# Kernel tuning notes

Hardware: AMD Instinct MI355X
Metric: run time of the kernel (lower is better)

Reference implementation:

```python
import jax, jax.numpy as jnp
import numpy as np

D_MODEL = 1024
D_STATE = 64
D_CONV = 4
EXPAND = 2
HEADDIM = 64  # Hydra default (config.headdim is not forwarded by the block)
D_INNER = EXPAND * D_MODEL            # 2048
NHEADS = D_INNER // HEADDIM           # 32
D_IN_PROJ = 2 * D_INNER + 2 * D_STATE + 2 * NHEADS  # 4288
CONV_DIM = D_INNER + 2 * D_STATE      # 2176
CHUNK = 64
EPS = 1e-5
BATCH, SEQLEN = 4, 2048


def setup_inputs() -> dict:
    key = jax.random.key(0)
    ks = jax.random.split(key, 8)
    w = lambda k, shape, s=0.02: (jax.random.normal(k, shape, jnp.float32) * s)
    dt = jnp.linspace(1e-3, 1e-1, NHEADS, dtype=jnp.float32)
    return {
        "hidden_states": jax.random.normal(ks[0], (BATCH, SEQLEN, D_MODEL), jnp.float32),
        "residual": jax.random.normal(ks[1], (BATCH, SEQLEN, D_MODEL), jnp.float32),
        "norm_weight": jnp.ones((D_MODEL,), jnp.float32),
        "in_proj_w": w(ks[2], (D_IN_PROJ, D_MODEL)),
        "conv_w": w(ks[3], (CONV_DIM, 1, D_CONV), 0.2),
        "conv_b": jnp.zeros((CONV_DIM,), jnp.float32),
        "dt_bias": jnp.log(jnp.expm1(dt)),  # inverse-softplus init, as in Mamba2/Hydra
        "A_log": jnp.log(jnp.linspace(1.0, 16.0, NHEADS, dtype=jnp.float32)),
        "D": jnp.ones((NHEADS,), jnp.float32),
        "fc_D_w": w(ks[4], (NHEADS, D_INNER)),
        "gn_weight": jnp.ones((D_INNER,), jnp.float32),
        "out_proj_w": w(ks[5], (D_MODEL, D_INNER)),
    }


def _rmsnorm(x, weight):
    x = x.astype(jnp.float32)
    return x * jax.lax.rsqrt(jnp.mean(x * x, axis=-1, keepdims=True) + EPS) * weight


def _segsum(x):
    # x: (..., T) -> lower-triangular cumulative segment sums, -inf above diag
    T = x.shape[-1]
    cs = jnp.cumsum(x, axis=-1)
    ss = cs[..., :, None] - cs[..., None, :]
    mask = jnp.tril(jnp.ones((T, T), bool))
    return jnp.where(mask, ss, -jnp.inf)


def _ssd(X, A, Bm, Cm, block):
    # Chunked SSD (mamba_chunk_scan_combined math, D=None, z=None, ngroups=1)
    # X: (b,l,h,p) = dt*x ; A: (b,l,h) = dt*A ; Bm, Cm: (b,l,n)
    b, l, h, p = X.shape
    c = l // block
    X = X.reshape(b, c, block, h, p)
    A = A.reshape(b, c, block, h).transpose(0, 3, 1, 2)          # (b,h,c,l)
    Bm = Bm.reshape(b, c, block, -1)
    Cm = Cm.reshape(b, c, block, -1)
    A_cum = jnp.cumsum(A, axis=-1)
    Lmat = jnp.exp(_segsum(A))                                   # (b,h,c,l,s)
    Y_diag = jnp.einsum("bcln,bcsn,bhcls,bcshp->bclhp", Cm, Bm, Lmat, X)
    decay = jnp.exp(A_cum[..., -1:] - A_cum)                     # (b,h,c,l)
    states = jnp.einsum("bcln,bhcl,bclhp->bchpn", Bm, decay, X)
    states = jnp.concatenate([jnp.zeros_like(states[:, :1]), states], axis=1)
    dchunk = jnp.exp(_segsum(jnp.pad(A_cum[..., -1], ((0, 0), (0, 0), (1, 0)))))
    states = jnp.einsum("bhzc,bchpn->bzhpn", dchunk, states)[:, :-1]
    Y_off = jnp.einsum("bcln,bchpn,bhcl->bclhp", Cm, states, jnp.exp(A_cum))
    return (Y_diag + Y_off).reshape(b, l, h, p)


def _hydra(h, in_proj_w, conv_w, conv_b, dt_bias, A_log, D, fc_D_w, gn_weight, out_proj_w):
    b, l, _ = h.shape
    zxbcdt = h @ in_proj_w.T                                     # (b,l,4288)
    z = zxbcdt[..., :D_INNER]
    xBC = zxbcdt[..., D_INNER:D_INNER + CONV_DIM]
    dt = zxbcdt[..., D_INNER + CONV_DIM:]                        # (b,l,2H)
    # fwd heads + time-flipped bwd heads, stacked on batch -> (2b,l,H)
    dt = jnp.concatenate([dt[..., :NHEADS], jnp.flip(dt[..., NHEADS:], axis=1)], axis=0)
    dt = jax.nn.softplus(dt + dt_bias)
    A = -jnp.exp(A_log)                                          # (H,)
    # causal depthwise conv, kernel D_CONV
    pad = jnp.pad(xBC, ((0, 0), (D_CONV - 1, 0), (0, 0)))
    conv = conv_b + sum(pad[:, k:k + l, :] * conv_w[:, 0, k] for k in range(D_CONV))
    xBC = jax.nn.silu(conv)
    x = xBC[..., :D_INNER]
    Bm = xBC[..., D_INNER:D_INNER + D_STATE]
    Cm = xBC[..., D_INNER + D_STATE:]
    x2 = jnp.concatenate([x, jnp.flip(x, axis=1)], axis=0)       # (2b,l,d_inner)
    B2 = jnp.concatenate([Bm, jnp.flip(Bm, axis=1)], axis=0)
    C2 = jnp.concatenate([Cm, jnp.flip(Cm, axis=1)], axis=0)
    X = x2.reshape(2 * b, l, NHEADS, HEADDIM) * dt[..., None]    # dt-discretized input
    y = _ssd(X, dt * A, B2, C2, CHUNK).reshape(2 * b, l, D_INNER)
    # quasiseparable combine: strict lower (shift fwd by +1) + strict upper + data-dep diag
    y = jnp.roll(y, 1, axis=1).at[:, 0, :].set(0.0)
    y = y[:b] + jnp.flip(y[b:], axis=1)
    Deff = x @ fc_D_w.T + D                                      # (b,l,H)
    y = y + x * jnp.repeat(Deff, HEADDIM, axis=-1)
    y = _rmsnorm(y * jax.nn.silu(z), gn_weight)                  # gated RMSNorm
    return y @ out_proj_w.T


def reference(hidden_states, residual, norm_weight, in_proj_w, conv_w, conv_b,
              dt_bias, A_log, D, fc_D_w, gn_weight, out_proj_w):
    res = (hidden_states + residual).astype(jnp.float32)         # residual_in_fp32
    h = _rmsnorm(res, norm_weight)                               # fused add+RMSNorm (prenorm)
    out = _hydra(h, in_proj_w, conv_w, conv_b, dt_bias, A_log, D, fc_D_w, gn_weight, out_proj_w)
    return out, res
```

## Files before the change

kernel.cpp:

```cpp
#include <hip/hip_runtime.h>

typedef __attribute__((ext_vector_type(4))) float f32x4;
typedef __attribute__((ext_vector_type(8))) short short8;
typedef __attribute__((ext_vector_type(8))) unsigned short ushort8;
typedef unsigned short u16;
typedef unsigned int u32;

#define DMODEL 1024
#define DINNER 2048
#define NH     32
#define DIP    4288
#define DIP_PAD 4352
#define CONVD  2176
#define LSEQ   2048
#define ROWS   8192
#define NCHUNK 32

static __device__ __forceinline__ float bf2f(u16 u) {
  u32 x = ((u32)u) << 16;
  return __builtin_bit_cast(float, x);
}
static __device__ __forceinline__ u16 f2bf(float f) {
  u32 x = __builtin_bit_cast(u32, f);
  x += 0x7fffu + ((x >> 16) & 1u);
  return (u16)(x >> 16);
}
static __device__ __forceinline__ f32x4 mfma16(short8 a, short8 b, f32x4 c) {
  return __builtin_amdgcn_mfma_f32_16x16x32_bf16(a, b, c, 0, 0, 0);
}

#define GLDS(gp, lp)                                                     \
  __builtin_amdgcn_global_load_lds(                                     \
      (const __attribute__((address_space(1))) void*)(gp),              \
      (__attribute__((address_space(3))) void*)(lp), 16, 0, 0)

__global__ __launch_bounds__(256) void k_cast(const float* __restrict__ s, u16* __restrict__ d) {
  size_t i = ((size_t)blockIdx.x * 256 + threadIdx.x) * 4;
  float4 v = *(const float4*)(s + i);
  u32 lo = (u32)f2bf(v.x) | ((u32)f2bf(v.y) << 16);
  u32 hi = (u32)f2bf(v.z) | ((u32)f2bf(v.w) << 16);
  *(uint2*)(d + i) = make_uint2(lo, hi);
}

__global__ __launch_bounds__(256) void k_addnorm(const float* __restrict__ h,
                                                 const float* __restrict__ r,
                                                 const float* __restrict__ nw,
                                                 float* __restrict__ res,
                                                 u16* __restrict__ hn) {
  int row = blockIdx.x, t = threadIdx.x;
  const float4* hp = (const float4*)(h + (size_t)row * DMODEL);
  const float4* rp = (const float4*)(r + (size_t)row * DMODEL);
  float4 a = hp[t], b = rp[t];
  float4 s;
  s.x = a.x + b.x; s.y = a.y + b.y; s.z = a.z + b.z; s.w = a.w + b.w;
  ((float4*)(res + (size_t)row * DMODEL))[t] = s;
  float ss = s.x * s.x + s.y * s.y + s.z * s.z + s.w * s.w;
  for (int m = 32; m; m >>= 1) ss += __shfl_xor(ss, m);
  __shared__ float wsum[4];
  if ((t & 63) == 0) wsum[t >> 6] = ss;
  __syncthreads();
  float tot = wsum[0] + wsum[1] + wsum[2] + wsum[3];
  float rinv = rsqrtf(tot * (1.0f / DMODEL) + 1e-5f);
  float4 w4 = ((const float4*)nw)[t];
  u32 lo = (u32)f2bf(s.x * rinv * w4.x) | ((u32)f2bf(s.y * rinv * w4.y) << 16);
  u32 hi = (u32)f2bf(s.z * rinv * w4.z) | ((u32)f2bf(s.w * rinv * w4.w) << 16);
  *(uint2*)(hn + (size_t)row * DMODEL + t * 4) = make_uint2(lo, hi);
}

template <int MODE>
__global__ __launch_bounds__(256) void k_gemm(const u16* __restrict__ A,
                                              const u16* __restrict__ Bw, int K, int nN,
                                              float* __restrict__ outf,
                                              u16* __restrict__ zb, u16* __restrict__ xb,
                                              float* __restrict__ dtp,
                                              const float* __restrict__ dt_bias) {
  constexpr int ABY = 128 * 64 * 2;
  constexpr int TB = 2 * ABY;
  __shared__ char lds[2 * TB];

  const int tid = threadIdx.x, wave = tid >> 6, lane = tid & 63;
  const int wm = wave >> 1, wn = wave & 1;
  const int lr = lane & 15, lg = lane >> 4;

  const int cpx = gridDim.x >> 3;
  const int orig = blockIdx.x;
  const int wg = (orig & 7) * cpx + (orig >> 3);
  const int brow = (wg / nN) * 128;
  const int bcol = (wg % nN) * 128;
  const int NK = K >> 6;

  size_t srcA[4], srcB[4];
#pragma unroll
  for (int g = 0; g < 4; ++g) {
    int d = g * 4096 + tid * 16;
    int s = d ^ (((d >> 7) & 7) << 4);
    srcA[g] = (size_t)(brow + (s >> 7)) * K + ((s & 127) >> 1);
    srcB[g] = (size_t)(bcol + (s >> 7)) * K + ((s & 127) >> 1);
  }

  auto STAGE = [&](int buf, int kt) {
    char* base = lds + buf * TB;
    size_t koff = (size_t)kt * 64;
#pragma unroll
    for (int g = 0; g < 4; ++g)
      GLDS(A + srcA[g] + koff, base + g * 4096 + wave * 1024);
#pragma unroll
    for (int g = 0; g < 4; ++g)
      GLDS(Bw + srcB[g] + koff, base + ABY + g * 4096 + wave * 1024);
  };

  int offA[4][2], offB[4][2];
#pragma unroll
  for (int i = 0; i < 4; ++i)
#pragma unroll
    for (int ks = 0; ks < 2; ++ks) {
      int rA = wm * 64 + i * 16 + lr;
      offA[i][ks] = (rA * 128 + ks * 64 + lg * 16) ^ ((lr & 7) << 4);
      int rB = wn * 64 + i * 16 + lr;
      offB[i][ks] = ABY + ((rB * 128 + ks * 64 + lg * 16) ^ ((lr & 7) << 4));
    }

  f32x4 acc[4][4] = {};
  STAGE(0, 0);
  asm volatile("s_waitcnt vmcnt(0)" ::: "memory");
  __builtin_amdgcn_s_barrier();
  for (int t = 0; t < NK; ++t) {
    const int cur = t & 1;
    if (t + 1 < NK) STAGE(cur ^ 1, t + 1);
    const char* bb = lds + cur * TB;
    short8 af[4], bfr[4];
#pragma unroll
    for (int i = 0; i < 4; ++i) af[i] = *(const short8*)(bb + offA[i][0]);
#pragma unroll
    for (int j = 0; j < 4; ++j) bfr[j] = *(const short8*)(bb + offB[j][0]);
    __builtin_amdgcn_s_setprio(1);
#pragma unroll
    for (int i = 0; i < 4; ++i)
#pragma unroll
      for (int j = 0; j < 4; ++j) acc[i][j] = mfma16(af[i], bfr[j], acc[i][j]);
    __builtin_amdgcn_s_setprio(0);
#pragma unroll
    for (int i = 0; i < 4; ++i) af[i] = *(const short8*)(bb + offA[i][1]);
#pragma unroll
    for (int j = 0; j < 4; ++j) bfr[j] = *(const short8*)(bb + offB[j][1]);
    __builtin_amdgcn_s_setprio(1);
#pragma unroll
    for (int i = 0; i < 4; ++i)
#pragma unroll
      for (int j = 0; j < 4; ++j) acc[i][j] = mfma16(af[i], bfr[j], acc[i][j]);
    __builtin_amdgcn_s_setprio(0);
    if (t + 1 < NK) {
      asm volatile("s_waitcnt vmcnt(0)" ::: "memory");
      __builtin_amdgcn_s_barrier();
    }
  }

  const int mb = brow + wm * 64 + lg * 4;
  const int nb = bcol + wn * 64 + lr;
#pragma unroll
  for (int i = 0; i < 4; ++i)
#pragma unroll
    for (int j = 0; j < 4; ++j)
#pragma unroll
      for (int rr = 0; rr < 4; ++rr) {
        int m = mb + i * 16 + rr;
        int n = nb + j * 16;
        float v = acc[i][j][rr];
        if constexpr (MODE == 1) {
          outf[(size_t)m * 1024 + n] = v;
        } else {
          if (n < DINNER) {
            zb[(size_t)m * DINNER + n] = f2bf(v);
          } else if (n < DINNER + CONVD) {
            xb[(size_t)m * CONVD + (n - DINNER)] = f2bf(v);
          } else if (n < DIP) {
            int h2 = n - (DINNER + CONVD);
            float uu = v + dt_bias[h2 & 31];
            float sp = (uu > 20.f) ? uu : log1pf(expf(uu));
            int bb2 = m >> 11, tt = m & 2047;
            int obb = bb2, ot = tt;
            if (h2 >= 32) { obb = bb2 + 4; ot = 2047 - tt; }
            dtp[((size_t)(obb << 11) + ot) * NH + (h2 & 31)] = sp;
          }
        }
      }
}

__global__ __launch_bounds__(256) void k_conv(const u16* __restrict__ xbc,
                                              const float* __restrict__ cw,
                                              const float* __restrict__ cb,
                                              u16* __restrict__ xc, u16* __restrict__ bm,
                                              u16* __restrict__ cm) {
  int e = blockIdx.x * 256 + threadIdx.x;
  int c8 = e % 272;
  int rq = e / 272;
  int b = rq >> 9;
  int t0 = (rq & 511) * 4;
  int c = c8 * 8;

  float4 w[8];
  float a[4][8];
#pragma unroll
  for (int j = 0; j < 8; ++j) {
    w[j] = *(const float4*)&cw[(c + j) * 4];
    float bias = cb[c + j];
#pragma unroll
    for (int i = 0; i < 4; ++i) a[i][j] = bias;
  }
  const u16* base = xbc + (size_t)(b << 11) * CONVD + c;
#pragma unroll
  for (int k = 0; k < 7; ++k) {
    int tt = t0 - 3 + k;
    if (tt >= 0) {
      ushort8 v = *(const ushort8*)(base + (size_t)tt * CONVD);
#pragma unroll
      for (int i = 0; i < 4; ++i) {
        int kk = k - i;
        if (kk >= 0 && kk < 4) {
#pragma unroll
          for (int j = 0; j < 8; ++j) a[i][j] += bf2f(v[j]) * ((const float*)&w[j])[kk];
        }
      }
    }
  }
#pragma unroll
  for (int i = 0; i < 4; ++i) {
    ushort8 o;
#pragma unroll
    for (int j = 0; j < 8; ++j) {
      float s = a[i][j] * (1.f / (1.f + expf(-a[i][j])));
      o[j] = f2bf(s);
    }
    size_t r = (size_t)(b << 11) + t0 + i;
    if (c8 < 256) *(ushort8*)(xc + r * DINNER + c) = o;
    else if (c8 < 264) *(ushort8*)(bm + r * 64 + (c - DINNER)) = o;
    else *(ushort8*)(cm + r * 64 + (c - DINNER - 64)) = o;
  }
}

__global__ __launch_bounds__(512) void k_ssd(const u16* __restrict__ xc,
                                             const u16* __restrict__ bmat,
                                             const u16* __restrict__ cmat,
                                             const float* __restrict__ dtp,
                                             const float* __restrict__ alog,
                                             u16* __restrict__ y0, u16* __restrict__ y1) {
  const int h = blockIdx.x & 31;
  const int grp = blockIdx.x >> 5;
  const int dir = grp >> 2;
  const int bt = grp & 3;
  const int tid = threadIdx.x, wave = tid >> 6, lane = tid & 63;
  const int lq = wave >> 1, wh = wave & 1;
  const int lr = lane & 15, lg = lane >> 4;
  const float Ah = -expf(alog[h]);

  __shared__ u16 sB[64][72];
  __shared__ u16 sC[64][72];
  __shared__ u16 sXM[64][72];
  __shared__ u16 sXT[64][72];
  __shared__ u16 sBT[64][72];
  __shared__ u16 sSb[64][72];
  __shared__ float sS[64][68];
  __shared__ float sAc[64], sEA[64], sSc[64], sDt[64];

  for (int i = tid; i < 64 * 64; i += 512) {
    sS[i >> 6][i & 63] = 0.f;
    sSb[i >> 6][i & 63] = 0;
  }

  const int srow = tid >> 3, q8 = (tid & 7) * 8;

  auto rowOf = [&](int c) {
    int tdir = c * 64 + srow;
    return bt * LSEQ + (dir ? (LSEQ - 1 - tdir) : tdir);
  };

  int rg = rowOf(0);
  ushort8 rB = *(const ushort8*)(bmat + (size_t)rg * 64 + q8);
  ushort8 rC = *(const ushort8*)(cmat + (size_t)rg * 64 + q8);
  ushort8 rX = *(const ushort8*)(xc + (size_t)rg * DINNER + h * 64 + q8);

  for (int c = 0; c < NCHUNK; ++c) {
    *(ushort8*)&sB[srow][q8] = rB;
    *(ushort8*)&sC[srow][q8] = rC;
    *(ushort8*)&sXM[srow][q8] = rX;
    __syncthreads();

    {
      ushort8 vx, vb;
#pragma unroll
      for (int i = 0; i < 8; ++i) {
        vx[i] = sXM[wave * 8 + i][lane];
        vb[i] = sB[wave * 8 + i][lane];
      }
      *(ushort8*)&sXT[lane][wave * 8] = vx;
      *(ushort8*)&sBT[lane][wave * 8] = vb;
    }
    if (wave == 0) {
      int s = lane;
      float dv = dtp[((size_t)grp * LSEQ + c * 64 + s) * NH + h];
      float a = dv * Ah;
      float x = a;
#pragma unroll
      for (int d = 1; d < 64; d <<= 1) {
        float y = __shfl_up(x, d);
        if (s >= d) x += y;
      }
      float tot = __shfl(x, 63);
      sAc[s] = x;
      sEA[s] = expf(x);
      sSc[s] = expf(tot - x) * dv;
      sDt[s] = dv;
    }
    __syncthreads();

    if (c + 1 < NCHUNK) {
      int rg2 = rowOf(c + 1);
      rB = *(const ushort8*)(bmat + (size_t)rg2 * 64 + q8);
      rC = *(const ushort8*)(cmat + (size_t)rg2 * 64 + q8);
      rX = *(const ushort8*)(xc + (size_t)rg2 * DINNER + h * 64 + q8);
    }

    f32x4 acc_y[2] = {};
    {
      f32x4 acc_g[2] = {};
#pragma unroll
      for (int ks = 0; ks < 2; ++ks) {
        int kof = ks * 32 + lg * 8;
        short8 af = *(const short8*)&sC[lq * 16 + lr][kof];
#pragma unroll
        for (int nt = 0; nt < 2; ++nt) {
          short8 bf = *(const short8*)&sB[wh * 32 + nt * 16 + lr][kof];
          acc_g[nt] = mfma16(af, bf, acc_g[nt]);
        }
      }
#pragma unroll
      for (int ks = 0; ks < 2; ++ks) {
        int kof = ks * 32 + lg * 8;
        short8 af = *(const short8*)&sC[lq * 16 + lr][kof];
#pragma unroll
        for (int nt = 0; nt < 2; ++nt) {
          short8 bf = *(const short8*)&sSb[wh * 32 + nt * 16 + lr][kof];
          acc_y[nt] = mfma16(af, bf, acc_y[nt]);
        }
      }
#pragma unroll
      for (int nt = 0; nt < 2; ++nt)
#pragma unroll
        for (int rr = 0; rr < 4; ++rr) {
          int l = lq * 16 + lg * 4 + rr;
          int s = wh * 32 + nt * 16 + lr;
          float g = acc_g[nt][rr];
          float m = (l >= s) ? g * sDt[s] * expf(sAc[l] - sAc[s]) : 0.f;
          sXM[l][s] = f2bf(m);
        }
    }
    __syncthreads();

#pragma unroll
    for (int nt = 0; nt < 2; ++nt)
#pragma unroll
      for (int rr = 0; rr < 4; ++rr) acc_y[nt][rr] *= sEA[lq * 16 + lg * 4 + rr];
#pragma unroll
    for (int ks = 0; ks < 2; ++ks) {
      int kof = ks * 32 + lg * 8;
      short8 af = *(const short8*)&sXM[lq * 16 + lr][kof];
#pragma unroll
      for (int nt = 0; nt < 2; ++nt) {
        short8 bf = *(const short8*)&sXT[wh * 32 + nt * 16 + lr][kof];
        acc_y[nt] = mfma16(af, bf, acc_y[nt]);
      }
    }
#pragma unroll
    for (int nt = 0; nt < 2; ++nt)
#pragma unroll
      for (int rr = 0; rr < 4; ++rr) {
        int l = lq * 16 + lg * 4 + rr;
        int p = wh * 32 + nt * 16 + lr;
        int tg = c * 64 + l;
        if (tg <= LSEQ - 2) {
          float v = acc_y[nt][rr];
          if (dir == 0)
            y0[((size_t)bt * LSEQ + tg + 1) * DINNER + h * 64 + p] = f2bf(v);
          else
            y1[((size_t)bt * LSEQ + (LSEQ - 2 - tg)) * DINNER + h * 64 + p] = f2bf(v);
        }
      }
    if (c == 0 && tid < 64) {
      if (dir == 0)
        y0[((size_t)bt * LSEQ) * DINNER + h * 64 + tid] = 0;
      else
        y1[((size_t)bt * LSEQ + (LSEQ - 1)) * DINNER + h * 64 + tid] = 0;
    }
    {
      f32x4 acc_s[2] = {};
#pragma unroll
      for (int ks = 0; ks < 2; ++ks) {
        int kof = ks * 32 + lg * 8;
        ushort8 xr = *(const ushort8*)&sXT[lq * 16 + lr][kof];
        short8 af;
#pragma unroll
        for (int e = 0; e < 8; ++e) af[e] = (short)f2bf(bf2f(xr[e]) * sSc[kof + e]);
#pragma unroll
        for (int nt = 0; nt < 2; ++nt) {
          short8 bf = *(const short8*)&sBT[wh * 32 + nt * 16 + lr][kof];
          acc_s[nt] = mfma16(af, bf, acc_s[nt]);
        }
      }
      float lam = sEA[63];
#pragma unroll
      for (int nt = 0; nt < 2; ++nt)
#pragma unroll
        for (int rr = 0; rr < 4; ++rr) {
          int p = lq * 16 + lg * 4 + rr;
          int n = wh * 32 + nt * 16 + lr;
          float ns = lam * sS[p][n] + acc_s[nt][rr];
          sS[p][n] = ns;
          sSb[p][n] = f2bf(ns);
        }
    }
    __syncthreads();
  }
}

__global__ __launch_bounds__(256) void k_deff(const u16* __restrict__ xcv,
                                              const u16* __restrict__ fwb,
                                              const float* __restrict__ Dv,
                                              float* __restrict__ deff) {
  __shared__ float red[2][64][8];
  const int tid = threadIdx.x, wave = tid >> 6, lane = tid & 63;
  const int lr = lane & 15, lg = lane >> 4;
  const int rowg = wave & 1;
  const int kg = wave >> 1;
  const int rb = blockIdx.x * 32 + rowg * 16;
  const u16* xrow = xcv + (size_t)(rb + lr) * DINNER + kg * 1024 + lg * 8;
  const u16* f0 = fwb + (size_t)lr * DINNER + kg * 1024 + lg * 8;
  const u16* f1 = fwb + (size_t)(16 + lr) * DINNER + kg * 1024 + lg * 8;
  f32x4 a0 = {}, a1 = {};
  for (int k = 0; k < 1024; k += 32) {
    short8 bf = *(const short8*)(xrow + k);
    short8 af0 = *(const short8*)(f0 + k);
    short8 af1 = *(const short8*)(f1 + k);
    a0 = mfma16(af0, bf, a0);
    a1 = mfma16(af1, bf, a1);
  }
  if (kg == 1) {
#pragma unroll
    for (int rr = 0; rr < 4; ++rr) {
      red[rowg][lane][rr] = a0[rr];
      red[rowg][lane][4 + rr] = a1[rr];
    }
  }
  __syncthreads();
  if (kg == 0) {
    float4 o0, o1;
#pragma unroll
    for (int rr = 0; rr < 4; ++rr) {
      ((float*)&o0)[rr] = a0[rr] + red[rowg][lane][rr] + Dv[lg * 4 + rr];
      ((float*)&o1)[rr] = a1[rr] + red[rowg][lane][4 + rr] + Dv[16 + lg * 4 + rr];
    }
    *(float4*)&deff[(size_t)(rb + lr) * NH + lg * 4] = o0;
    *(float4*)&deff[(size_t)(rb + lr) * NH + 16 + lg * 4] = o1;
  }
}

__global__ __launch_bounds__(256) void k_gate(const u16* __restrict__ yb0,
                                              const u16* __restrict__ yb1,
                                              const u16* __restrict__ xcv,
                                              const float* __restrict__ deff,
                                              const u16* __restrict__ zb,
                                              const float* __restrict__ gnw,
                                              u16* __restrict__ yn) {
  int row = blockIdx.x, t = threadIdx.x;
  size_t base = (size_t)row * DINNER + t * 8;
  ushort8 y0v = *(const ushort8*)(yb0 + base);
  ushort8 y1v = *(const ushort8*)(yb1 + base);
  ushort8 xv = *(const ushort8*)(xcv + base);
  ushort8 zv = *(const ushort8*)(zb + base);
  float de = deff[row * NH + (t >> 3)];
  float g[8];
  float ss = 0.f;
#pragma unroll
  for (int j = 0; j < 8; ++j) {
    float y = bf2f(y0v[j]) + bf2f(y1v[j]) + bf2f(xv[j]) * de;
    float z = bf2f(zv[j]);
    float gg = y * (z / (1.f + expf(-z)));
    g[j] = gg;
    ss += gg * gg;
  }
  for (int m = 32; m; m >>= 1) ss += __shfl_xor(ss, m);
  __shared__ float wsum[4];
  if ((t & 63) == 0) wsum[t >> 6] = ss;
  __syncthreads();
  float tot = wsum[0] + wsum[1] + wsum[2] + wsum[3];
  float rinv = rsqrtf(tot * (1.0f / DINNER) + 1e-5f);
  u32 w0 = (u32)f2bf(g[0] * rinv * gnw[t * 8 + 0]) | ((u32)f2bf(g[1] * rinv * gnw[t * 8 + 1]) << 16);
  u32 w1 = (u32)f2bf(g[2] * rinv * gnw[t * 8 + 2]) | ((u32)f2bf(g[3] * rinv * gnw[t * 8 + 3]) << 16);
  u32 w2 = (u32)f2bf(g[4] * rinv * gnw[t * 8 + 4]) | ((u32)f2bf(g[5] * rinv * gnw[t * 8 + 5]) << 16);
  u32 w3 = (u32)f2bf(g[6] * rinv * gnw[t * 8 + 6]) | ((u32)f2bf(g[7] * rinv * gnw[t * 8 + 7]) << 16);
  *(uint4*)(yn + base) = make_uint4(w0, w1, w2, w3);
}

extern "C" void kernel_launch(void* const* d_in, const int* in_sizes, int n_in,
                              void* d_out, int out_size, void* d_ws, size_t ws_size,
                              hipStream_t stream) {
  (void)in_sizes; (void)n_in; (void)out_size; (void)ws_size;
  const float* hid = (const float*)d_in[0];
  const float* resin = (const float*)d_in[1];
  const float* nw = (const float*)d_in[2];
  const float* w1 = (const float*)d_in[3];
  const float* cw = (const float*)d_in[4];
  const float* cb = (const float*)d_in[5];
  const float* dtb = (const float*)d_in[6];
  const float* alog = (const float*)d_in[7];
  const float* Dv = (const float*)d_in[8];
  const float* fcw = (const float*)d_in[9];
  const float* gnw = (const float*)d_in[10];
  const float* w2 = (const float*)d_in[11];
  float* out = (float*)d_out;
  float* resout = out + (size_t)ROWS * DMODEL;

  char* ws = (char*)d_ws;
  size_t o = 0;
  auto alloc = [&](size_t bytes) {
    char* p = ws + o;
    o += (bytes + 255) & ~(size_t)255;
    return p;
  };
  u16* W1b = (u16*)alloc((size_t)DIP_PAD * DMODEL * 2);
  u16* HN = (u16*)alloc((size_t)ROWS * DMODEL * 2);
  u16* XBC = (u16*)alloc((size_t)ROWS * CONVD * 2);
  u16* ZB = (u16*)alloc((size_t)ROWS * DINNER * 2);
  u16* XC = (u16*)alloc((size_t)ROWS * DINNER * 2);
  u16* BM = (u16*)alloc((size_t)ROWS * 64 * 2);
  u16* CM = (u16*)alloc((size_t)ROWS * 64 * 2);
  float* DT = (float*)alloc((size_t)8 * LSEQ * NH * 4);
  float* DE = (float*)alloc((size_t)ROWS * NH * 4);
  u16* FWB = (u16*)alloc((size_t)NH * DINNER * 2);
  u16* YB0 = XBC;
  u16* YB1 = (u16*)out;
  u16* W2b = W1b;
  u16* YN = HN;

  k_cast<<<(DIP * DMODEL) / 1024, 256, 0, stream>>>(w1, W1b);
  k_addnorm<<<ROWS, 256, 0, stream>>>(hid, resin, nw, resout, HN);
  k_gemm<0><<<64 * 34, 256, 0, stream>>>(HN, W1b, DMODEL, 34, nullptr, ZB, XBC, DT, dtb);
  k_conv<<<(ROWS / 4) * 272 / 256, 256, 0, stream>>>(XBC, cw, cb, XC, BM, CM);
  k_ssd<<<256, 512, 0, stream>>>(XC, BM, CM, DT, alog, YB0, YB1);
  k_cast<<<(DMODEL * DINNER) / 1024, 256, 0, stream>>>(w2, W2b);
  k_cast<<<(NH * DINNER) / 1024, 256, 0, stream>>>(fcw, FWB);
  k_deff<<<ROWS / 32, 256, 0, stream>>>(XC, FWB, Dv, DE);
  k_gate<<<ROWS, 256, 0, stream>>>(YB0, YB1, XC, DE, ZB, gnw, YN);
  k_gemm<1><<<64 * 8, 256, 0, stream>>>(YN, W2b, DINNER, 8, out, nullptr, nullptr, nullptr,
                                        nullptr);
}
```

Measured before the change: 412.9 us.

## Use 256x256-tile, 8-wave GEMM for the input projection

Adds a dedicated in_proj GEMM kernel with 256x256 output tiles, 512 threads and 128KB LDS double buffering. The K-tile is split into two halves, and loads for the next tile are interleaved with MFMA phases. The larger tile raises arithmetic intensity and cuts global/LDS traffic per FLOP. The cost is a single block per CU and fewer blocks overall (544), which can hurt tail balance and latency hiding. The out_proj GEMM keeps the old 128x128 kernel, now specialized to the fp32 output path.

```diff
diff --git a/kernel.cpp b/kernel.cpp
--- a/kernel.cpp
+++ b/kernel.cpp
@@ -67,13 +67,157 @@
   *(uint2*)(hn + (size_t)row * DMODEL + t * 4) = make_uint2(lo, hi);
 }
 
-template <int MODE>
+__global__ __launch_bounds__(512) void k_gemm256(const u16* __restrict__ A,
+                                                 const u16* __restrict__ Bw, int K, int nN,
+                                                 u16* __restrict__ zb, u16* __restrict__ xb,
+                                                 float* __restrict__ dtp,
+                                                 const float* __restrict__ dt_bias) {
+  __shared__ char lds[131072];
+  const int tid = threadIdx.x, wave = tid >> 6, lane = tid & 63;
+  const int wm = wave >> 2, wn = wave & 3;
+  const int lr = lane & 15, lg = lane >> 4;
+
+  const int cpx = gridDim.x >> 3;
+  const int orig = blockIdx.x;
+  const int wg = (orig & 7) * cpx + (orig >> 3);
+  const int brow = (wg / nN) * 256;
+  const int bcol = (wg % nN) * 256;
+  const int NT = K >> 6;
+
+  size_t srcA[2], srcB[2];
+#pragma unroll
+  for (int g = 0; g < 2; ++g) {
+    int d = g * 8192 + tid * 16;
+    int r = d >> 6;
+    int q = ((d >> 4) & 3) ^ (r & 3);
+    srcA[g] = (size_t)(brow + r) * K + q * 8;
+    srcB[g] = (size_t)(bcol + r) * K + q * 8;
+  }
+
+  auto STAGE_A = [&](int buf, int kh, int kt) {
+    char* dst = lds + buf * 65536 + kh * 16384 + wave * 1024;
+    size_t koff = (size_t)kt * 64 + kh * 32;
+    GLDS(A + srcA[0] + koff, dst);
+    GLDS(A + srcA[1] + koff, dst + 8192);
+  };
+  auto STAGE_B = [&](int buf, int kh, int kt) {
+    char* dst = lds + buf * 65536 + 32768 + kh * 16384 + wave * 1024;
+    size_t koff = (size_t)kt * 64 + kh * 32;
+    GLDS(Bw + srcB[0] + koff, dst);
+    GLDS(Bw + srcB[1] + koff, dst + 8192);
+  };
+
+  int offA[8], offB[4];
+#pragma unroll
+  for (int i = 0; i < 8; ++i) {
+    int row = wm * 128 + i * 16 + lr;
+    offA[i] = row * 64 + ((lg * 16) ^ ((row & 3) << 4));
+  }
+#pragma unroll
+  for (int j = 0; j < 4; ++j) {
+    int row = wn * 64 + j * 16 + lr;
+    offB[j] = 32768 + row * 64 + ((lg * 16) ^ ((row & 3) << 4));
+  }
+
+  f32x4 acc[8][4] = {};
+  STAGE_A(0, 0, 0);
+  STAGE_B(0, 0, 0);
+  STAGE_A(0, 1, 0);
+  STAGE_B(0, 1, 0);
+
+  for (int t = 0; t < NT; ++t) {
+    const int cb = t & 1, nb = cb ^ 1;
+    const char* rb = lds + cb * 65536;
+    short8 af[8], b0, b1;
+    asm volatile("s_waitcnt vmcnt(4)" ::: "memory");
+    __builtin_amdgcn_s_barrier();
+    __builtin_amdgcn_sched_barrier(0);
+#pragma unroll
+    for (int i = 0; i < 8; ++i) af[i] = *(const short8*)(rb + offA[i]);
+    b0 = *(const short8*)(rb + offB[0]);
+    b1 = *(const short8*)(rb + offB[1]);
+    if (t + 1 < NT) STAGE_A(nb, 0, t + 1);
+    __builtin_amdgcn_s_setprio(1);
+#pragma unroll
+    for (int i = 0; i < 8; ++i) {
+      acc[i][0] = mfma16(af[i], b0, acc[i][0]);
+      acc[i][1] = mfma16(af[i], b1, acc[i][1]);
+    }
+    __builtin_amdgcn_s_setprio(0);
+    __builtin_amdgcn_sched_barrier(0);
+    b0 = *(const short8*)(rb + offB[2]);
+    b1 = *(const short8*)(rb + offB[3]);
+    if (t + 1 < NT) STAGE_B(nb, 0, t + 1);
+    __builtin_amdgcn_s_setprio(1);
+#pragma unroll
+    for (int i = 0; i < 8; ++i) {
+      acc[i][2] = mfma16(af[i], b0, acc[i][2]);
+      acc[i][3] = mfma16(af[i], b1, acc[i][3]);
+    }
+    __builtin_amdgcn_s_setprio(0);
+    __builtin_amdgcn_sched_barrier(0);
+    if (t + 1 < NT)
+      asm volatile("s_waitcnt vmcnt(4)" ::: "memory");
+    else
+      asm volatile("s_waitcnt vmcnt(0)" ::: "memory");
+    __builtin_amdgcn_s_barrier();
+    __builtin_amdgcn_sched_barrier(0);
+#pragma unroll
+    for (int i = 0; i < 8; ++i) af[i] = *(const short8*)(rb + 16384 + offA[i]);
+    b0 = *(const short8*)(rb + 16384 + offB[0]);
+    b1 = *(const short8*)(rb + 16384 + offB[1]);
+    if (t + 1 < NT) STAGE_A(nb, 1, t + 1);
+    __builtin_amdgcn_s_setprio(1);
+#pragma unroll
+    for (int i = 0; i < 8; ++i) {
+      acc[i][0] = mfma16(af[i], b0, acc[i][0]);
+      acc[i][1] = mfma16(af[i], b1, acc[i][1]);
+    }
+    __builtin_amdgcn_s_setprio(0);
+    __builtin_amdgcn_sched_barrier(0);
+    b0 = *(const short8*)(rb + 16384 + offB[2]);
+    b1 = *(const short8*)(rb + 16384 + offB[3]);
+    if (t + 1 < NT) STAGE_B(nb, 1, t + 1);
+    __builtin_amdgcn_s_setprio(1);
+#pragma unroll
+    for (int i = 0; i < 8; ++i) {
+      acc[i][2] = mfma16(af[i], b0, acc[i][2]);
+      acc[i][3] = mfma16(af[i], b1, acc[i][3]);
+    }
+    __builtin_amdgcn_s_setprio(0);
+    __builtin_amdgcn_sched_barrier(0);
+  }
+
+  const int mb = brow + wm * 128 + lg * 4;
+  const int nb2 = bcol + wn * 64 + lr;
+#pragma unroll
+  for (int i = 0; i < 8; ++i)
+#pragma unroll
+    for (int j = 0; j < 4; ++j)
+#pragma unroll
+      for (int rr = 0; rr < 4; ++rr) {
+        int m = mb + i * 16 + rr;
+        int n = nb2 + j * 16;
+        float v = acc[i][j][rr];
+        if (n < DINNER) {
+          zb[(size_t)m * DINNER + n] = f2bf(v);
+        } else if (n < DINNER + CONVD) {
+          xb[(size_t)m * CONVD + (n - DINNER)] = f2bf(v);
+        } else if (n < DIP) {
+          int h2 = n - (DINNER + CONVD);
+          float uu = v + dt_bias[h2 & 31];
+          float sp = (uu > 20.f) ? uu : log1pf(expf(uu));
+          int bb2 = m >> 11, tt = m & 2047;
+          int obb = bb2, ot = tt;
+          if (h2 >= 32) { obb = bb2 + 4; ot = 2047 - tt; }
+          dtp[((size_t)(obb << 11) + ot) * NH + (h2 & 31)] = sp;
+        }
+      }
+}
+
 __global__ __launch_bounds__(256) void k_gemm(const u16* __restrict__ A,
                                               const u16* __restrict__ Bw, int K, int nN,
-                                              float* __restrict__ outf,
-                                              u16* __restrict__ zb, u16* __restrict__ xb,
-                                              float* __restrict__ dtp,
-                                              const float* __restrict__ dt_bias) {
+                                              float* __restrict__ outf) {
   constexpr int ABY = 128 * 64 * 2;
   constexpr int TB = 2 * ABY;
   __shared__ char lds[2 * TB];
@@ -165,24 +309,7 @@
       for (int rr = 0; rr < 4; ++rr) {
         int m = mb + i * 16 + rr;
         int n = nb + j * 16;
-        float v = acc[i][j][rr];
-        if constexpr (MODE == 1) {
-          outf[(size_t)m * 1024 + n] = v;
-        } else {
-          if (n < DINNER) {
-            zb[(size_t)m * DINNER + n] = f2bf(v);
-          } else if (n < DINNER + CONVD) {
-            xb[(size_t)m * CONVD + (n - DINNER)] = f2bf(v);
-          } else if (n < DIP) {
-            int h2 = n - (DINNER + CONVD);
-            float uu = v + dt_bias[h2 & 31];
-            float sp = (uu > 20.f) ? uu : log1pf(expf(uu));
-            int bb2 = m >> 11, tt = m & 2047;
-            int obb = bb2, ot = tt;
-            if (h2 >= 32) { obb = bb2 + 4; ot = 2047 - tt; }
-            dtp[((size_t)(obb << 11) + ot) * NH + (h2 & 31)] = sp;
-          }
-        }
+        outf[(size_t)m * 1024 + n] = acc[i][j][rr];
       }
 }
 
@@ -543,13 +670,12 @@
 
   k_cast<<<(DIP * DMODEL) / 1024, 256, 0, stream>>>(w1, W1b);
   k_addnorm<<<ROWS, 256, 0, stream>>>(hid, resin, nw, resout, HN);
-  k_gemm<0><<<64 * 34, 256, 0, stream>>>(HN, W1b, DMODEL, 34, nullptr, ZB, XBC, DT, dtb);
+  k_gemm256<<<32 * 17, 512, 0, stream>>>(HN, W1b, DMODEL, 17, ZB, XBC, DT, dtb);
   k_conv<<<(ROWS / 4) * 272 / 256, 256, 0, stream>>>(XBC, cw, cb, XC, BM, CM);
   k_ssd<<<256, 512, 0, stream>>>(XC, BM, CM, DT, alog, YB0, YB1);
   k_cast<<<(DMODEL * DINNER) / 1024, 256, 0, stream>>>(w2, W2b);
   k_cast<<<(NH * DINNER) / 1024, 256, 0, stream>>>(fcw, FWB);
   k_deff<<<ROWS / 32, 256, 0, stream>>>(XC, FWB, Dv, DE);
   k_gate<<<ROWS, 256, 0, stream>>>(YB0, YB1, XC, DE, ZB, gnw, YN);
-  k_gemm<1><<<64 * 8, 256, 0, stream>>>(YN, W2b, DINNER, 8, out, nullptr, nullptr, nullptr,
-                                        nullptr);
-}
+  k_gemm<<<64 * 8, 256, 0, stream>>>(YN, W2b, DINNER, 8, out);
+}
```

After: 539.1 us. +30.6%, slower.
